# Optimization experiments

Measured on AMD Instinct MI355X. Metric: run time of the kernel, lower is better.

## Reference

```python
import jax, jax.numpy as jnp
import numpy as np

DECAY = 0.99
EPS = 1e-5
COMMITMENT_COST = 0.25


def setup_inputs() -> dict:
    key = jax.random.key(0)
    k1, k2, k3, k4 = jax.random.split(key, 4)
    N, D, K = 262144, 128, 512
    return {
        "z": jax.random.normal(k1, (N, D), dtype=jnp.float32),
        "embedding": jax.random.normal(k2, (K, D), dtype=jnp.float32),
        "ema_cluster_size": jax.random.uniform(k3, (K,), dtype=jnp.float32),
        "ema_w": jax.random.normal(k4, (K, D), dtype=jnp.float32),
    }


def reference(z, embedding, ema_cluster_size, ema_w):
    # EMA-based VectorQuantizer forward (training mode), matching torch source.
    D = z.shape[-1]
    K = embedding.shape[0]
    flat_z = z.reshape(-1, D)  # [N, D]

    # ||z||^2 + ||e||^2 - 2 z.e  -> [N, K]
    distances = (
        jnp.sum(flat_z * flat_z, axis=1, keepdims=True)
        + jnp.sum(embedding * embedding, axis=1)
        - 2.0 * flat_z @ embedding.T
    )
    indices = jnp.argmin(distances, axis=1)  # [N]

    # one_hot @ embedding == gather (same math, no dense [N,K] one-hot)
    z_q = embedding[indices]  # [N, D]

    # EMA buffer updates (torch does these on buffers / .data, no grads)
    counts = jax.ops.segment_sum(jnp.ones_like(indices, dtype=flat_z.dtype), indices, num_segments=K)
    new_ema_cluster_size = ema_cluster_size * DECAY + (1.0 - DECAY) * counts
    dw = jax.ops.segment_sum(flat_z, indices, num_segments=K)  # encodings.T @ flat_z
    new_ema_w = ema_w * DECAY + (1.0 - DECAY) * dw
    n = jnp.sum(new_ema_cluster_size)
    cluster_size = (new_ema_cluster_size + EPS) / (n + K * EPS) * n
    new_embedding = new_ema_w / cluster_size[:, None]

    loss = COMMITMENT_COST * jnp.mean((jax.lax.stop_gradient(z_q) - flat_z) ** 2)
    # straight-through estimator
    z_q_st = flat_z + jax.lax.stop_gradient(z_q - flat_z)
    z_q_st = z_q_st.reshape(z.shape)
    return (z_q_st, loss, indices, new_ema_cluster_size, new_ema_w, new_embedding)
```

## Files before the change

kernel.cpp:

```cpp
#include <hip/hip_runtime.h>

#define NPTS 262144
#define DIM 128
#define KCL 512

constexpr float DECAY = 0.99f;
constexpr float EPSV = 1e-5f;
constexpr float CCOST = 0.25f;

#define O_ZQ 0
#define O_LOSS (NPTS * DIM)
#define O_IDX (O_LOSS + 1)
#define O_NECS (O_IDX + NPTS)
#define O_NEMAW (O_NECS + KCL)
#define O_NEMB (O_NEMAW + KCL * DIM)

#define W_ENORM 0
#define W_COUNTS 512
#define W_LOSS 1024
#define W_NFLAG 1025
#define W_DW 1088
#define W_CS 66624
#define W_OFF 67136
#define W_CUR 67712
#define W_EHI 68224
#define W_ELO 100992
#define W_FLAG 133760
#define FLAGCAP 32768
#define W_IDX 199296
#define W_SORTED (W_IDX + NPTS)

#define MARGIN 0.005f
#define SEG 64

using v8h = __attribute__((ext_vector_type(8))) _Float16;
using v4f = __attribute__((ext_vector_type(4))) float;

__global__ void k_enorm(const float* __restrict__ emb, float* __restrict__ wsf) {
    int k = blockIdx.x * blockDim.x + threadIdx.x;
    if (k < KCL) {
        const float4* row = (const float4*)(emb + (size_t)k * DIM);
        float s = 0.0f;
#pragma unroll
        for (int i = 0; i < DIM / 4; i++) {
            float4 v = row[i];
            s += v.x * v.x + v.y * v.y + v.z * v.z + v.w * v.w;
        }
        wsf[W_ENORM + k] = s;
    }
}

__global__ void k_prep(const float* __restrict__ emb,
                       unsigned short* __restrict__ ehi,
                       unsigned short* __restrict__ elo) {
    int gi = blockIdx.x * 256 + threadIdx.x;
    int lane = gi & 63, ks = (gi >> 6) & 3, g = gi >> 8;
    int col = lane & 15, quad = lane >> 4;
    const float* src = emb + (size_t)(g * 16 + col) * DIM + ks * 32 + quad * 8;
    float4 a = *(const float4*)src;
    float4 b = *(const float4*)(src + 4);
    float f[8] = {a.x, a.y, a.z, a.w, b.x, b.y, b.z, b.w};
    union { unsigned short s[8]; int4 v; } uh, ul;
#pragma unroll
    for (int j = 0; j < 8; j++) {
        _Float16 h = (_Float16)f[j];
        float r = f[j] - (float)h;
        _Float16 l = (_Float16)r;
        uh.s[j] = __builtin_bit_cast(unsigned short, h);
        ul.s[j] = __builtin_bit_cast(unsigned short, l);
    }
    *(int4*)&ehi[(size_t)gi * 8] = uh.v;
    *(int4*)&elo[(size_t)gi * 8] = ul.v;
}

__global__ __launch_bounds__(256, 3) void k_main(
    const float* __restrict__ z, const float* __restrict__ emb,
    const unsigned short* __restrict__ ehi, const unsigned short* __restrict__ elo,
    float* __restrict__ out, float* __restrict__ wsf,
    unsigned* __restrict__ wsu, int* __restrict__ wsi) {
    __shared__ short seh[8192];
    __shared__ short sel[8192];
    __shared__ float sen[KCL];
    __shared__ float m1v[64];
    __shared__ int   m1i[64];
    __shared__ float m2v[64];
    __shared__ int   ishs[64];

    const int t = threadIdx.x;
    const int blk = blockIdx.x;
    const int w = t >> 6;
    const int lane = t & 63;
    const int col = lane & 15;
    const int quad = lane >> 4;
    const int wrow = w & 1;
    const int wcol = w >> 1;

    sen[t] = wsf[W_ENORM + t];
    sen[t + 256] = wsf[W_ENORM + t + 256];

    v8h ah[2][4], al[2][4];
    float zn[2];
#pragma unroll
    for (int mt = 0; mt < 2; mt++) {
        zn[mt] = 0.0f;
        const float* zr = z + (size_t)(blk * 64 + wrow * 32 + mt * 16 + col) * DIM;
#pragma unroll
        for (int ks = 0; ks < 4; ks++) {
            const float* p = zr + ks * 32 + quad * 8;
            float4 a = *(const float4*)p;
            float4 b = *(const float4*)(p + 4);
            float f[8] = {a.x, a.y, a.z, a.w, b.x, b.y, b.z, b.w};
#pragma unroll
            for (int j = 0; j < 8; j++) {
                _Float16 h = (_Float16)f[j];
                float r = f[j] - (float)h;
                ah[mt][ks][j] = h;
                al[mt][ks][j] = (_Float16)r;
                zn[mt] += f[j] * f[j];
            }
        }
        zn[mt] += __shfl_xor(zn[mt], 16);
        zn[mt] += __shfl_xor(zn[mt], 32);
    }

    float rv1[8], rv2[8];
    int ri1[8];
#pragma unroll
    for (int s = 0; s < 8; s++) { rv1[s] = 3.4e38f; rv2[s] = 3.4e38f; ri1[s] = 0; }

    for (int kt = 0; kt < 8; kt++) {
        __syncthreads();
        {
            const int4* srch = (const int4*)(ehi + (size_t)kt * 8192);
            const int4* srcl = (const int4*)(elo + (size_t)kt * 8192);
#pragma unroll
            for (int i = 0; i < 4; i++) {
                int idx = t + 256 * i;
                ((int4*)seh)[idx] = srch[idx];
                ((int4*)sel)[idx] = srcl[idx];
            }
        }
        __syncthreads();

        v4f acc[2][2];
#pragma unroll
        for (int mt = 0; mt < 2; mt++)
#pragma unroll
            for (int nt = 0; nt < 2; nt++) { v4f zz = {0.f, 0.f, 0.f, 0.f}; acc[mt][nt] = zz; }

#pragma unroll
        for (int ks = 0; ks < 4; ks++) {
            v8h bh[2], bl[2];
#pragma unroll
            for (int nt = 0; nt < 2; nt++) {
                int off = ((wcol * 2 + nt) * 4 + ks) * 512 + lane * 8;
                bh[nt] = *(const v8h*)&seh[off];
                bl[nt] = *(const v8h*)&sel[off];
            }
#pragma unroll
            for (int nt = 0; nt < 2; nt++)
#pragma unroll
                for (int mt = 0; mt < 2; mt++)
                    acc[mt][nt] = __builtin_amdgcn_mfma_f32_16x16x32_f16(ah[mt][ks], bh[nt], acc[mt][nt], 0, 0, 0);
#pragma unroll
            for (int nt = 0; nt < 2; nt++)
#pragma unroll
                for (int mt = 0; mt < 2; mt++)
                    acc[mt][nt] = __builtin_amdgcn_mfma_f32_16x16x32_f16(al[mt][ks], bh[nt], acc[mt][nt], 0, 0, 0);
#pragma unroll
            for (int nt = 0; nt < 2; nt++)
#pragma unroll
                for (int mt = 0; mt < 2; mt++)
                    acc[mt][nt] = __builtin_amdgcn_mfma_f32_16x16x32_f16(ah[mt][ks], bl[nt], acc[mt][nt], 0, 0, 0);
        }

#pragma unroll
        for (int nt = 0; nt < 2; nt++) {
            int kbase = kt * 64 + wcol * 32 + nt * 16 + col;
            float en = sen[kbase];
#pragma unroll
            for (int mt = 0; mt < 2; mt++)
#pragma unroll
                for (int r = 0; r < 4; r++) {
                    int s = mt * 4 + r;
                    float dist = en - 2.0f * acc[mt][nt][r];
                    if (dist < rv1[s]) { rv2[s] = rv1[s]; rv1[s] = dist; ri1[s] = kbase; }
                    else if (dist < rv2[s]) rv2[s] = dist;
                }
        }
    }

#pragma unroll
    for (int m = 1; m < 16; m <<= 1) {
#pragma unroll
        for (int s = 0; s < 8; s++) {
            float c1 = __shfl_xor(rv1[s], m);
            int ci1 = __shfl_xor(ri1[s], m);
            float c2 = __shfl_xor(rv2[s], m);
            if (c1 < rv1[s] || (c1 == rv1[s] && ci1 < ri1[s])) {
                rv2[s] = fminf(rv1[s], c2);
                rv1[s] = c1; ri1[s] = ci1;
            } else {
                rv2[s] = fminf(rv2[s], c1);
            }
        }
    }

    float znp[8];
#pragma unroll
    for (int s = 0; s < 8; s++) znp[s] = __shfl(zn[s >> 2], quad * 4 + (s & 3));

    if (wcol == 0 && col == 0) {
#pragma unroll
        for (int s = 0; s < 8; s++) {
            int p = wrow * 32 + (s >> 2) * 16 + quad * 4 + (s & 3);
            m1v[p] = rv1[s]; m1i[p] = ri1[s]; m2v[p] = rv2[s];
        }
    }
    __syncthreads();
    float lossacc = 0.0f;
    if (wcol == 1 && col == 0) {
#pragma unroll
        for (int s = 0; s < 8; s++) {
            int p = wrow * 32 + (s >> 2) * 16 + quad * 4 + (s & 3);
            float a1 = m1v[p]; int ai1 = m1i[p]; float a2 = m2v[p];
            float v1, v2; int i1;
            if (a1 < rv1[s] || (a1 == rv1[s] && ai1 < ri1[s])) {
                v1 = a1; i1 = ai1; v2 = fminf(a2, rv1[s]);
            } else {
                v1 = rv1[s]; i1 = ri1[s]; v2 = fminf(rv2[s], a1);
            }
            float fd = v1 + znp[s];
            int gp = blk * 64 + p;
            out[O_IDX + gp] = (float)i1;
            wsi[W_IDX + gp] = i1;
            ishs[p] = i1;
            atomicAdd(&wsu[W_COUNTS + i1], 1u);
            lossacc += fd;
            if (v2 - v1 < MARGIN) {
                unsigned pos = atomicAdd(&wsu[W_NFLAG], 1u);
                if (pos < FLAGCAP) {
                    wsu[W_FLAG + 2 * pos] = (unsigned)gp;
                    wsu[W_FLAG + 2 * pos + 1] = __float_as_uint(fd);
                }
            }
        }
    }
    for (int o = 32; o > 0; o >>= 1) lossacc += __shfl_down(lossacc, o);
    if (lane == 0) atomicAdd(&wsf[W_LOSS], lossacc);

    __syncthreads();
    float* outz = out + (size_t)blk * 64 * DIM;
#pragma unroll
    for (int i = 0; i < 8; i++) {
        int f4 = t + 256 * i;
        int p = f4 >> 5, dq = f4 & 31;
        int ci = ishs[p];
        float4 v = *(const float4*)(emb + (size_t)ci * DIM + 4 * dq);
        *((float4*)outz + f4) = v;
    }
}

__global__ __launch_bounds__(256) void k_recheck(
    const float* __restrict__ z, const float* __restrict__ emb,
    float* __restrict__ out, float* __restrict__ wsf,
    unsigned* __restrict__ wsu, int* __restrict__ wsi) {
    __shared__ float zrow[DIM];
    __shared__ double sd[256];
    __shared__ int si[256];
    __shared__ int schg, snew;
    const int t = threadIdx.x;
    unsigned nf = wsu[W_NFLAG];
    if (nf > FLAGCAP) nf = FLAGCAP;
    for (unsigned fi = blockIdx.x; fi < nf; fi += gridDim.x) {
        unsigned gp = wsu[W_FLAG + 2 * fi];
        float fd_prov = __uint_as_float(wsu[W_FLAG + 2 * fi + 1]);
        __syncthreads();
        if (t < DIM) zrow[t] = z[(size_t)gp * DIM + t];
        __syncthreads();
        double best = 1e300; int bi = 0;
        for (int c = t; c < KCL; c += 256) {
            const float* er = emb + (size_t)c * DIM;
            double d = 0.0;
            for (int dd = 0; dd < DIM; dd++) {
                double df = (double)zrow[dd] - (double)er[dd];
                d += df * df;
            }
            if (d < best) { best = d; bi = c; }
        }
        sd[t] = best; si[t] = bi;
        __syncthreads();
        for (int o = 128; o > 0; o >>= 1) {
            if (t < o) {
                if (sd[t + o] < sd[t] || (sd[t + o] == sd[t] && si[t + o] < si[t])) {
                    sd[t] = sd[t + o]; si[t] = si[t + o];
                }
            }
            __syncthreads();
        }
        if (t == 0) {
            int inew = si[0];
            int iold = wsi[W_IDX + gp];
            snew = inew;
            schg = (inew != iold);
            atomicAdd(&wsf[W_LOSS], (float)sd[0] - fd_prov);
            if (inew != iold) {
                wsi[W_IDX + gp] = inew;
                out[O_IDX + gp] = (float)inew;
                atomicAdd(&wsu[W_COUNTS + iold], (unsigned)-1);
                atomicAdd(&wsu[W_COUNTS + inew], 1u);
            }
        }
        __syncthreads();
        if (schg && t < DIM) out[(size_t)gp * DIM + t] = emb[(size_t)snew * DIM + t];
        __syncthreads();
    }
}

__global__ void k_finalize(const float* __restrict__ ema_cs, float* __restrict__ out,
                           float* __restrict__ wsf, unsigned* __restrict__ wsu) {
    __shared__ float s[KCL];
    __shared__ unsigned sc[KCL];
    int t = threadIdx.x;
    unsigned c = wsu[W_COUNTS + t];
    float necs = ema_cs[t] * DECAY + (1.0f - DECAY) * (float)c;
    out[O_NECS + t] = necs;
    s[t] = necs;
    __syncthreads();
    for (int o = 256; o > 0; o >>= 1) {
        if (t < o) s[t] += s[t + o];
        __syncthreads();
    }
    float n = s[0];
    float cs = (necs + EPSV) / (n + (float)KCL * EPSV) * n;
    wsf[W_CS + t] = cs;
    sc[t] = c;
    __syncthreads();
    for (int o = 1; o < KCL; o <<= 1) {
        unsigned v = (t >= o) ? sc[t - o] : 0u;
        __syncthreads();
        sc[t] += v;
        __syncthreads();
    }
    unsigned excl = sc[t] - c;
    wsu[W_OFF + t] = excl;
    wsu[W_CUR + t] = excl;
    if (t == 0) {
        out[O_LOSS] = CCOST * wsf[W_LOSS] / (float)((size_t)NPTS * DIM);
        wsu[W_OFF + KCL] = NPTS;
    }
}

__global__ void k_scatter(unsigned* __restrict__ wsu, const int* __restrict__ wsi) {
    int p = blockIdx.x * blockDim.x + threadIdx.x;
    int k = wsi[W_IDX + p];
    unsigned pos = atomicAdd(&wsu[W_CUR + k], 1u);
    wsu[W_SORTED + pos] = (unsigned)p;
}

__global__ __launch_bounds__(256) void k_dwseg(
    const float* __restrict__ z, float* __restrict__ wsf,
    const unsigned* __restrict__ wsu) {
    __shared__ unsigned soff[KCL + 1];
    __shared__ unsigned sidx[SEG];
    const int t = threadIdx.x;
    for (int i = t; i < KCL + 1; i += 256) soff[i] = wsu[W_OFF + i];
    const int base = blockIdx.x * SEG;
    if (t < SEG) sidx[t] = wsu[W_SORTED + base + t];
    __syncthreads();

    const int r = t >> 7;
    const int d = t & 127;
    const int pos0 = base + r;
    int lo = 0, hi = KCL;
    while (lo < hi) {
        int mid = (lo + hi + 1) >> 1;
        if (soff[mid] <= (unsigned)pos0) lo = mid; else hi = mid - 1;
    }
    int curk = lo;
    float acc = 0.0f;
#pragma unroll 4
    for (int j = 0; j < SEG / 2; j++) {
        int pos = pos0 + 2 * j;
        unsigned p = sidx[pos - base];
        while ((unsigned)pos >= soff[curk + 1]) {
            if (acc != 0.0f) atomicAdd(&wsf[W_DW + curk * DIM + d], acc);
            acc = 0.0f;
            curk++;
        }
        acc += z[(size_t)p * DIM + d];
    }
    atomicAdd(&wsf[W_DW + curk * DIM + d], acc);
}

__global__ void k_emb(const float* __restrict__ ema_w, float* __restrict__ out,
                      const float* __restrict__ wsf) {
    int i = blockIdx.x * 256 + threadIdx.x;
    int k = i >> 7;
    float dw = wsf[W_DW + i];
    float nw = ema_w[i] * DECAY + (1.0f - DECAY) * dw;
    out[O_NEMAW + i] = nw;
    out[O_NEMB + i] = nw / wsf[W_CS + k];
}

extern "C" void kernel_launch(void* const* d_in, const int* in_sizes, int n_in,
                              void* d_out, int out_size, void* d_ws, size_t ws_size,
                              hipStream_t stream) {
    const float* z = (const float*)d_in[0];
    const float* emb = (const float*)d_in[1];
    const float* ema_cs = (const float*)d_in[2];
    const float* ema_w = (const float*)d_in[3];
    float* out = (float*)d_out;
    float* wsf = (float*)d_ws;
    unsigned* wsu = (unsigned*)d_ws;
    int* wsi = (int*)d_ws;
    unsigned short* ehi = (unsigned short*)(wsu + W_EHI);
    unsigned short* elo = (unsigned short*)(wsu + W_ELO);

    hipMemsetAsync((char*)d_ws + (size_t)W_COUNTS * 4, 0,
                   (size_t)(W_DW + KCL * DIM - W_COUNTS) * 4, stream);

    k_enorm<<<2, 256, 0, stream>>>(emb, wsf);
    k_prep<<<32, 256, 0, stream>>>(emb, ehi, elo);
    k_main<<<NPTS / 64, 256, 0, stream>>>(z, emb, ehi, elo, out, wsf, wsu, wsi);
    k_recheck<<<1024, 256, 0, stream>>>(z, emb, out, wsf, wsu, wsi);
    k_finalize<<<1, KCL, 0, stream>>>(ema_cs, out, wsf, wsu);
    k_scatter<<<NPTS / 256, 256, 0, stream>>>(wsu, wsi);
    k_dwseg<<<NPTS / SEG, 256, 0, stream>>>(z, wsf, wsu);
    k_emb<<<KCL * DIM / 256, 256, 0, stream>>>(ema_w, out, wsf);
}
```

Before: 809.4 us.

## Drop low-half embedding split, widen tiles, add two-stage fp32 recheck

The main distance kernel stops using the fp16 low part of the codebook, which removes one third of the MFMAs. Each block now covers 256 points with 512 threads and keeps the whole fp16 codebook in shared memory, so the per-tile reloads and barriers go away. The wider margin that results from the lower precision is handled by a new batched fp32 recheck kernel, which passes only near-ties on to the existing double-precision recheck. Embedding norms are folded into the prep kernel. In exchange, many more points get flagged for recheck, the 128KB shared buffer limits occupancy, and results depend on the flag capacities being large enough.

```diff
diff --git a/kernel.cpp b/kernel.cpp
--- a/kernel.cpp
+++ b/kernel.cpp
@@ -19,72 +19,64 @@
 #define W_COUNTS 512
 #define W_LOSS 1024
 #define W_NFLAG 1025
+#define W_NFLAG2 1026
 #define W_DW 1088
 #define W_CS 66624
 #define W_OFF 67136
 #define W_CUR 67712
 #define W_EHI 68224
-#define W_ELO 100992
-#define W_FLAG 133760
-#define FLAGCAP 32768
+#define W_FLAG2 100992
+#define FLAG2CAP 4096
+#define W_FLAG 109184
+#define FLAGCAP 45056
 #define W_IDX 199296
 #define W_SORTED (W_IDX + NPTS)
 
-#define MARGIN 0.005f
+#define MARGIN 0.25f
+#define MARGIN2 0.005f
 #define SEG 64
+#define RB 16
 
 using v8h = __attribute__((ext_vector_type(8))) _Float16;
 using v4f = __attribute__((ext_vector_type(4))) float;
 
-__global__ void k_enorm(const float* __restrict__ emb, float* __restrict__ wsf) {
-    int k = blockIdx.x * blockDim.x + threadIdx.x;
-    if (k < KCL) {
-        const float4* row = (const float4*)(emb + (size_t)k * DIM);
-        float s = 0.0f;
-#pragma unroll
-        for (int i = 0; i < DIM / 4; i++) {
-            float4 v = row[i];
-            s += v.x * v.x + v.y * v.y + v.z * v.z + v.w * v.w;
-        }
-        wsf[W_ENORM + k] = s;
-    }
-}
-
 __global__ void k_prep(const float* __restrict__ emb,
                        unsigned short* __restrict__ ehi,
-                       unsigned short* __restrict__ elo) {
-    int gi = blockIdx.x * 256 + threadIdx.x;
-    int lane = gi & 63, ks = (gi >> 6) & 3, g = gi >> 8;
-    int col = lane & 15, quad = lane >> 4;
+                       float* __restrict__ wsf) {
+    __shared__ float part[4][16];
+    const int t = threadIdx.x;
+    const int g = blockIdx.x;
+    const int lane = t & 63, ks = t >> 6;
+    const int col = lane & 15, quad = lane >> 4;
     const float* src = emb + (size_t)(g * 16 + col) * DIM + ks * 32 + quad * 8;
     float4 a = *(const float4*)src;
     float4 b = *(const float4*)(src + 4);
     float f[8] = {a.x, a.y, a.z, a.w, b.x, b.y, b.z, b.w};
-    union { unsigned short s[8]; int4 v; } uh, ul;
+    union { unsigned short s[8]; int4 v; } uh;
+    float s2 = 0.0f;
 #pragma unroll
     for (int j = 0; j < 8; j++) {
         _Float16 h = (_Float16)f[j];
-        float r = f[j] - (float)h;
-        _Float16 l = (_Float16)r;
         uh.s[j] = __builtin_bit_cast(unsigned short, h);
-        ul.s[j] = __builtin_bit_cast(unsigned short, l);
-    }
-    *(int4*)&ehi[(size_t)gi * 8] = uh.v;
-    *(int4*)&elo[(size_t)gi * 8] = ul.v;
-}
-
-__global__ __launch_bounds__(256, 3) void k_main(
+        s2 += f[j] * f[j];
+    }
+    *(int4*)&ehi[((size_t)g * 256 + t) * 8] = uh.v;
+    s2 += __shfl_xor(s2, 16);
+    s2 += __shfl_xor(s2, 32);
+    if (quad == 0) part[ks][col] = s2;
+    __syncthreads();
+    if (t < 16)
+        wsf[W_ENORM + g * 16 + t] = part[0][t] + part[1][t] + part[2][t] + part[3][t];
+}
+
+__global__ __launch_bounds__(512, 2) void k_main(
     const float* __restrict__ z, const float* __restrict__ emb,
-    const unsigned short* __restrict__ ehi, const unsigned short* __restrict__ elo,
+    const unsigned short* __restrict__ ehi,
     float* __restrict__ out, float* __restrict__ wsf,
     unsigned* __restrict__ wsu, int* __restrict__ wsi) {
-    __shared__ short seh[8192];
-    __shared__ short sel[8192];
+    __shared__ short seh[KCL * DIM];
     __shared__ float sen[KCL];
-    __shared__ float m1v[64];
-    __shared__ int   m1i[64];
-    __shared__ float m2v[64];
-    __shared__ int   ishs[64];
+    __shared__ int   ishs[256];
 
     const int t = threadIdx.x;
     const int blk = blockIdx.x;
@@ -92,18 +84,21 @@
     const int lane = t & 63;
     const int col = lane & 15;
     const int quad = lane >> 4;
-    const int wrow = w & 1;
-    const int wcol = w >> 1;
-
+
+    int4 stg[16];
+    {
+        const int4* src = (const int4*)ehi;
+#pragma unroll
+        for (int i = 0; i < 16; i++) stg[i] = src[t + 512 * i];
+    }
     sen[t] = wsf[W_ENORM + t];
-    sen[t + 256] = wsf[W_ENORM + t + 256];
 
     v8h ah[2][4], al[2][4];
     float zn[2];
 #pragma unroll
     for (int mt = 0; mt < 2; mt++) {
         zn[mt] = 0.0f;
-        const float* zr = z + (size_t)(blk * 64 + wrow * 32 + mt * 16 + col) * DIM;
+        const float* zr = z + (size_t)(blk * 256 + w * 32 + mt * 16 + col) * DIM;
 #pragma unroll
         for (int ks = 0; ks < 4; ks++) {
             const float* p = zr + ks * 32 + quad * 8;
@@ -123,71 +118,45 @@
         zn[mt] += __shfl_xor(zn[mt], 32);
     }
 
+#pragma unroll
+    for (int i = 0; i < 16; i++) ((int4*)seh)[t + 512 * i] = stg[i];
+    __syncthreads();
+
     float rv1[8], rv2[8];
     int ri1[8];
 #pragma unroll
     for (int s = 0; s < 8; s++) { rv1[s] = 3.4e38f; rv2[s] = 3.4e38f; ri1[s] = 0; }
 
-    for (int kt = 0; kt < 8; kt++) {
-        __syncthreads();
-        {
-            const int4* srch = (const int4*)(ehi + (size_t)kt * 8192);
-            const int4* srcl = (const int4*)(elo + (size_t)kt * 8192);
-#pragma unroll
-            for (int i = 0; i < 4; i++) {
-                int idx = t + 256 * i;
-                ((int4*)seh)[idx] = srch[idx];
-                ((int4*)sel)[idx] = srcl[idx];
-            }
-        }
-        __syncthreads();
-
-        v4f acc[2][2];
+#pragma unroll 2
+    for (int g = 0; g < 32; g++) {
+        v8h bh[4];
+#pragma unroll
+        for (int ks = 0; ks < 4; ks++)
+            bh[ks] = *(const v8h*)&seh[((g * 4 + ks) * 64 + lane) * 8];
+        v4f acc0 = {0.f, 0.f, 0.f, 0.f}, acc1 = {0.f, 0.f, 0.f, 0.f};
+#pragma unroll
+        for (int ks = 0; ks < 4; ks++) {
+            acc0 = __builtin_amdgcn_mfma_f32_16x16x32_f16(ah[0][ks], bh[ks], acc0, 0, 0, 0);
+            acc1 = __builtin_amdgcn_mfma_f32_16x16x32_f16(ah[1][ks], bh[ks], acc1, 0, 0, 0);
+        }
+#pragma unroll
+        for (int ks = 0; ks < 4; ks++) {
+            acc0 = __builtin_amdgcn_mfma_f32_16x16x32_f16(al[0][ks], bh[ks], acc0, 0, 0, 0);
+            acc1 = __builtin_amdgcn_mfma_f32_16x16x32_f16(al[1][ks], bh[ks], acc1, 0, 0, 0);
+        }
+        const int kbase = g * 16 + col;
+        const float en = sen[kbase];
 #pragma unroll
         for (int mt = 0; mt < 2; mt++)
 #pragma unroll
-            for (int nt = 0; nt < 2; nt++) { v4f zz = {0.f, 0.f, 0.f, 0.f}; acc[mt][nt] = zz; }
-
-#pragma unroll
-        for (int ks = 0; ks < 4; ks++) {
-            v8h bh[2], bl[2];
-#pragma unroll
-            for (int nt = 0; nt < 2; nt++) {
-                int off = ((wcol * 2 + nt) * 4 + ks) * 512 + lane * 8;
-                bh[nt] = *(const v8h*)&seh[off];
-                bl[nt] = *(const v8h*)&sel[off];
-            }
-#pragma unroll
-            for (int nt = 0; nt < 2; nt++)
-#pragma unroll
-                for (int mt = 0; mt < 2; mt++)
-                    acc[mt][nt] = __builtin_amdgcn_mfma_f32_16x16x32_f16(ah[mt][ks], bh[nt], acc[mt][nt], 0, 0, 0);
-#pragma unroll
-            for (int nt = 0; nt < 2; nt++)
-#pragma unroll
-                for (int mt = 0; mt < 2; mt++)
-                    acc[mt][nt] = __builtin_amdgcn_mfma_f32_16x16x32_f16(al[mt][ks], bh[nt], acc[mt][nt], 0, 0, 0);
-#pragma unroll
-            for (int nt = 0; nt < 2; nt++)
-#pragma unroll
-                for (int mt = 0; mt < 2; mt++)
-                    acc[mt][nt] = __builtin_amdgcn_mfma_f32_16x16x32_f16(ah[mt][ks], bl[nt], acc[mt][nt], 0, 0, 0);
-        }
-
-#pragma unroll
-        for (int nt = 0; nt < 2; nt++) {
-            int kbase = kt * 64 + wcol * 32 + nt * 16 + col;
-            float en = sen[kbase];
-#pragma unroll
-            for (int mt = 0; mt < 2; mt++)
-#pragma unroll
-                for (int r = 0; r < 4; r++) {
-                    int s = mt * 4 + r;
-                    float dist = en - 2.0f * acc[mt][nt][r];
-                    if (dist < rv1[s]) { rv2[s] = rv1[s]; rv1[s] = dist; ri1[s] = kbase; }
-                    else if (dist < rv2[s]) rv2[s] = dist;
-                }
-        }
+            for (int r = 0; r < 4; r++) {
+                int s = mt * 4 + r;
+                float dist = fmaf(-2.0f, (mt ? acc1[r] : acc0[r]), en);
+                bool better = dist < rv1[s];
+                rv2[s] = fminf(fmaxf(dist, rv1[s]), rv2[s]);
+                rv1[s] = better ? dist : rv1[s];
+                ri1[s] = better ? kbase : ri1[s];
+            }
     }
 
 #pragma unroll
@@ -210,34 +179,20 @@
 #pragma unroll
     for (int s = 0; s < 8; s++) znp[s] = __shfl(zn[s >> 2], quad * 4 + (s & 3));
 
-    if (wcol == 0 && col == 0) {
+    float lossacc = 0.0f;
+    if (col == 0) {
 #pragma unroll
         for (int s = 0; s < 8; s++) {
-            int p = wrow * 32 + (s >> 2) * 16 + quad * 4 + (s & 3);
-            m1v[p] = rv1[s]; m1i[p] = ri1[s]; m2v[p] = rv2[s];
-        }
-    }
-    __syncthreads();
-    float lossacc = 0.0f;
-    if (wcol == 1 && col == 0) {
-#pragma unroll
-        for (int s = 0; s < 8; s++) {
-            int p = wrow * 32 + (s >> 2) * 16 + quad * 4 + (s & 3);
-            float a1 = m1v[p]; int ai1 = m1i[p]; float a2 = m2v[p];
-            float v1, v2; int i1;
-            if (a1 < rv1[s] || (a1 == rv1[s] && ai1 < ri1[s])) {
-                v1 = a1; i1 = ai1; v2 = fminf(a2, rv1[s]);
-            } else {
-                v1 = rv1[s]; i1 = ri1[s]; v2 = fminf(rv2[s], a1);
-            }
+            int p = w * 32 + (s >> 2) * 16 + quad * 4 + (s & 3);
+            int gp = blk * 256 + p;
+            float v1 = rv1[s]; int i1 = ri1[s];
             float fd = v1 + znp[s];
-            int gp = blk * 64 + p;
             out[O_IDX + gp] = (float)i1;
             wsi[W_IDX + gp] = i1;
             ishs[p] = i1;
             atomicAdd(&wsu[W_COUNTS + i1], 1u);
             lossacc += fd;
-            if (v2 - v1 < MARGIN) {
+            if (rv2[s] - v1 < MARGIN) {
                 unsigned pos = atomicAdd(&wsu[W_NFLAG], 1u);
                 if (pos < FLAGCAP) {
                     wsu[W_FLAG + 2 * pos] = (unsigned)gp;
@@ -250,18 +205,137 @@
     if (lane == 0) atomicAdd(&wsf[W_LOSS], lossacc);
 
     __syncthreads();
-    float* outz = out + (size_t)blk * 64 * DIM;
-#pragma unroll
-    for (int i = 0; i < 8; i++) {
-        int f4 = t + 256 * i;
+    float* outz = out + (size_t)blk * 256 * DIM;
+#pragma unroll
+    for (int i = 0; i < 16; i++) {
+        int f4 = t + 512 * i;
         int p = f4 >> 5, dq = f4 & 31;
         int ci = ishs[p];
         float4 v = *(const float4*)(emb + (size_t)ci * DIM + 4 * dq);
-        *((float4*)outz + f4) = v;
-    }
-}
-
-__global__ __launch_bounds__(256) void k_recheck(
+        ((float4*)outz)[f4] = v;
+    }
+}
+
+__global__ __launch_bounds__(256) void k_recheck1(
+    const float* __restrict__ z, const float* __restrict__ emb,
+    float* __restrict__ out, float* __restrict__ wsf,
+    unsigned* __restrict__ wsu, int* __restrict__ wsi) {
+    __shared__ float zs[RB][DIM];
+    __shared__ float zns[RB];
+    __shared__ unsigned sgp[RB];
+    __shared__ float sfd[RB];
+    __shared__ float r1[RB][257];
+    __shared__ float r2[RB][257];
+    __shared__ int   rix[RB][257];
+    const int t = threadIdx.x;
+    unsigned nf = wsu[W_NFLAG];
+    if (nf > FLAGCAP) nf = FLAGCAP;
+    unsigned nb = (nf + RB - 1) / RB;
+    for (unsigned b = blockIdx.x; b < nb; b += gridDim.x) {
+        __syncthreads();
+        if (t < RB) {
+            unsigned fi = b * RB + t;
+            if (fi < nf) {
+                sgp[t] = wsu[W_FLAG + 2 * fi];
+                sfd[t] = __uint_as_float(wsu[W_FLAG + 2 * fi + 1]);
+            } else { sgp[t] = 0u; sfd[t] = 0.0f; }
+        }
+        __syncthreads();
+        {
+            int p = t >> 4, j = t & 15;
+            const float4* src = (const float4*)(z + (size_t)sgp[p] * DIM);
+            *(float4*)&zs[p][j * 8] = src[j * 2];
+            *(float4*)&zs[p][j * 8 + 4] = src[j * 2 + 1];
+        }
+        __syncthreads();
+        if (t < RB) {
+            float s = 0.0f;
+            for (int d = 0; d < DIM; d += 4) {
+                float4 v = *(const float4*)&zs[t][d];
+                s += v.x * v.x + v.y * v.y + v.z * v.z + v.w * v.w;
+            }
+            zns[t] = s;
+        }
+        float acc0[RB], acc1[RB];
+#pragma unroll
+        for (int p = 0; p < RB; p++) { acc0[p] = 0.0f; acc1[p] = 0.0f; }
+        const float4* e0 = (const float4*)(emb + (size_t)(2 * t) * DIM);
+        const float4* e1 = (const float4*)(emb + (size_t)(2 * t + 1) * DIM);
+#pragma unroll 2
+        for (int ch = 0; ch < 32; ch++) {
+            float4 ea = e0[ch], eb = e1[ch];
+#pragma unroll
+            for (int p = 0; p < RB; p++) {
+                float4 zv = *(const float4*)&zs[p][ch * 4];
+                acc0[p] = fmaf(zv.x, ea.x, fmaf(zv.y, ea.y, fmaf(zv.z, ea.z, fmaf(zv.w, ea.w, acc0[p]))));
+                acc1[p] = fmaf(zv.x, eb.x, fmaf(zv.y, eb.y, fmaf(zv.z, eb.z, fmaf(zv.w, eb.w, acc1[p]))));
+            }
+        }
+        float en0 = wsf[W_ENORM + 2 * t];
+        float en1 = wsf[W_ENORM + 2 * t + 1];
+#pragma unroll
+        for (int p = 0; p < RB; p++) {
+            float d0 = fmaf(-2.0f, acc0[p], en0);
+            float d1 = fmaf(-2.0f, acc1[p], en1);
+            float v1 = d0, v2 = d1; int i1 = 2 * t;
+            if (d1 < d0) { v1 = d1; i1 = 2 * t + 1; v2 = d0; }
+            r1[p][t] = v1; rix[p][t] = i1; r2[p][t] = v2;
+        }
+        __syncthreads();
+        {
+            int p = t >> 4, j = t & 15;
+            float v1 = 3.4e38f, v2 = 3.4e38f; int i1 = 0x7fffffff;
+#pragma unroll
+            for (int k = 0; k < 16; k++) {
+                int idx = j + 16 * k;
+                float c1 = r1[p][idx]; int ci = rix[p][idx]; float c2 = r2[p][idx];
+                if (c1 < v1 || (c1 == v1 && ci < i1)) { v2 = fminf(v1, c2); v1 = c1; i1 = ci; }
+                else v2 = fminf(v2, c1);
+            }
+#pragma unroll
+            for (int m = 1; m < 16; m <<= 1) {
+                float c1 = __shfl_xor(v1, m);
+                int ci = __shfl_xor(i1, m);
+                float c2 = __shfl_xor(v2, m);
+                if (c1 < v1 || (c1 == v1 && ci < i1)) { v2 = fminf(v1, c2); v1 = c1; i1 = ci; }
+                else v2 = fminf(v2, c1);
+            }
+            bool valid = (b * RB + (unsigned)p < nf);
+            unsigned gp = sgp[p];
+            int chg = 0;
+            if (j == 0 && valid) {
+                if (v2 - v1 < MARGIN2) {
+                    unsigned pos = atomicAdd(&wsu[W_NFLAG2], 1u);
+                    if (pos < FLAG2CAP) {
+                        wsu[W_FLAG2 + 2 * pos] = gp;
+                        wsu[W_FLAG2 + 2 * pos + 1] = __float_as_uint(sfd[p]);
+                    }
+                } else {
+                    float d = v1 + zns[p];
+                    atomicAdd(&wsf[W_LOSS], d - sfd[p]);
+                    int iold = wsi[W_IDX + gp];
+                    if (i1 != iold) {
+                        chg = 1;
+                        wsi[W_IDX + gp] = i1;
+                        out[O_IDX + gp] = (float)i1;
+                        atomicAdd(&wsu[W_COUNTS + iold], (unsigned)-1);
+                        atomicAdd(&wsu[W_COUNTS + i1], 1u);
+                    }
+                }
+            }
+            chg = __shfl(chg, (t & 63) & ~15);
+            if (chg) {
+                int dd = j * 8;
+                *(float4*)&out[(size_t)gp * DIM + dd] =
+                    *(const float4*)&emb[(size_t)i1 * DIM + dd];
+                *(float4*)&out[(size_t)gp * DIM + dd + 4] =
+                    *(const float4*)&emb[(size_t)i1 * DIM + dd + 4];
+            }
+        }
+    }
+}
+
+__global__ __launch_bounds__(256) void k_recheck2(
     const float* __restrict__ z, const float* __restrict__ emb,
     float* __restrict__ out, float* __restrict__ wsf,
     unsigned* __restrict__ wsu, int* __restrict__ wsi) {
@@ -270,11 +344,11 @@
     __shared__ int si[256];
     __shared__ int schg, snew;
     const int t = threadIdx.x;
-    unsigned nf = wsu[W_NFLAG];
-    if (nf > FLAGCAP) nf = FLAGCAP;
+    unsigned nf = wsu[W_NFLAG2];
+    if (nf > FLAG2CAP) nf = FLAG2CAP;
     for (unsigned fi = blockIdx.x; fi < nf; fi += gridDim.x) {
-        unsigned gp = wsu[W_FLAG + 2 * fi];
-        float fd_prov = __uint_as_float(wsu[W_FLAG + 2 * fi + 1]);
+        unsigned gp = wsu[W_FLAG2 + 2 * fi];
+        float fd_prov = __uint_as_float(wsu[W_FLAG2 + 2 * fi + 1]);
         __syncthreads();
         if (t < DIM) zrow[t] = z[(size_t)gp * DIM + t];
         __syncthreads();
@@ -415,15 +489,14 @@
     unsigned* wsu = (unsigned*)d_ws;
     int* wsi = (int*)d_ws;
     unsigned short* ehi = (unsigned short*)(wsu + W_EHI);
-    unsigned short* elo = (unsigned short*)(wsu + W_ELO);
 
     hipMemsetAsync((char*)d_ws + (size_t)W_COUNTS * 4, 0,
                    (size_t)(W_DW + KCL * DIM - W_COUNTS) * 4, stream);
 
-    k_enorm<<<2, 256, 0, stream>>>(emb, wsf);
-    k_prep<<<32, 256, 0, stream>>>(emb, ehi, elo);
-    k_main<<<NPTS / 64, 256, 0, stream>>>(z, emb, ehi, elo, out, wsf, wsu, wsi);
-    k_recheck<<<1024, 256, 0, stream>>>(z, emb, out, wsf, wsu, wsi);
+    k_prep<<<32, 256, 0, stream>>>(emb, ehi, wsf);
+    k_main<<<NPTS / 256, 512, 0, stream>>>(z, emb, ehi, out, wsf, wsu, wsi);
+    k_recheck1<<<512, 256, 0, stream>>>(z, emb, out, wsf, wsu, wsi);
+    k_recheck2<<<256, 256, 0, stream>>>(z, emb, out, wsf, wsu, wsi);
     k_finalize<<<1, KCL, 0, stream>>>(ema_cs, out, wsf, wsu);
     k_scatter<<<NPTS / 256, 256, 0, stream>>>(wsu, wsi);
     k_dwseg<<<NPTS / SEG, 256, 0, stream>>>(z, wsf, wsu);
```

New measurement: 843.9 us. 1.04x slower.
